# Optimization experiments

Measured on AMD Instinct MI355X. Metric: run time of the kernel, lower is better.

Reference implementation:

```python
import jax, jax.numpy as jnp
import numpy as np

B = 32      # batch
N = 1024    # input_size (= maxval)
EPS = 1.0   # regularization_strength


def _isotonic_l2(y):
    """Non-increasing isotonic regression (L2) of each row of y: [B, n].

    Uses the minimax characterization  sol_i = min_{j<=i} max_{k>=i} mean(y[j..k]),
    which equals the PAV solution and yields the correct block-averaging Jacobian
    under autodiff. O(n^2) memory per row, fully vectorized.
    """
    b, n = y.shape
    cs = jnp.concatenate([jnp.zeros((b, 1), y.dtype), jnp.cumsum(y, axis=-1)], axis=-1)  # [B, n+1]
    j = jnp.arange(n)[:, None]   # start index
    k = jnp.arange(n)[None, :]   # end index
    length = (k - j + 1).astype(y.dtype)
    # M[b, j, k] = mean(y[b, j..k]) for k >= j
    M = (cs[:, None, 1:] - cs[:, :-1, None]) / jnp.where(k >= j, length, jnp.ones_like(length))
    M = jnp.where(k >= j, M, -jnp.inf)
    # Amax[b, j, i] = max_{k >= i} M[b, j, k]  (suffix max along k)
    Amax = jax.lax.cummax(M, axis=2, reverse=True)
    # restrict to j <= i, then minimize over j
    Amax = jnp.where(j <= k, Amax, jnp.inf)  # here the k-axis plays the role of i
    return jnp.min(Amax, axis=1)  # [B, n]


def _soft_rank(x, eps):
    """fast-soft-sort soft_rank, direction=ASCENDING, regularization='l2'."""
    b, n = x.shape
    theta = x / eps
    perm = jnp.argsort(-theta, axis=-1)                 # descending sort permutation
    s = jnp.take_along_axis(theta, perm, axis=-1)       # sorted (descending)
    w = jnp.arange(n, 0, -1, dtype=x.dtype)             # [n, n-1, ..., 1]
    sol = _isotonic_l2(s - w)                           # dual solution
    primal = s - sol                                    # projection, sorted order
    inv = jnp.argsort(perm, axis=-1)
    return jnp.take_along_axis(primal, inv, axis=-1)    # unpermute -> ranks in [1, n]


def setup_inputs() -> dict:
    key = jax.random.key(0)
    x = jax.random.normal(key, (B, N), dtype=jnp.float32)
    return {"x": x}


def reference(x) -> jnp.ndarray:
    ranks = _soft_rank(x, EPS)                          # [B, n]
    n = x.shape[1]
    t = jnp.arange(1, n + 1, dtype=x.dtype)             # rank targets 1..n
    # out[b, j, i] = relu(1 - |ranks[b, j] - (i + 1)|)  (== torch .permute(0, 2, 1) result)
    return jax.nn.relu(1.0 - jnp.abs(ranks[:, :, None] - t[None, None, :]))
```

## Files before the change

### kernel.cpp

```cpp
#include <hip/hip_runtime.h>
#include <stdint.h>

#define N 1024
#define BATCH 32
#define NFILL 2048

__global__ __launch_bounds__(256) void fused_kernel(const float* __restrict__ x,
                                                    float* __restrict__ out,
                                                    float* __restrict__ ranks) {
    if (blockIdx.x >= BATCH) {
        const int fid = blockIdx.x - BATCH;
        float4* o = reinterpret_cast<float4*>(out) + (size_t)fid * 4096 + threadIdx.x;
        const float4 z = make_float4(0.0f, 0.0f, 0.0f, 0.0f);
        #pragma unroll
        for (int i = 0; i < 16; ++i)
            o[i * 256] = z;
        return;
    }

    __shared__ double   regA[N];
    __shared__ float    regB[N];
    __shared__ uint16_t segid[N];
    __shared__ uint16_t run_start[N+1];
    __shared__ double   stk_sum[N];
    __shared__ uint32_t stk_cr[N];
    __shared__ double   wsumD[4];
    __shared__ int      wsumI[4];

    uint64_t* keys     = reinterpret_cast<uint64_t*>(regA);
    double*   csum     = regA;
    float*    ss       = regB;
    float*    yv       = regB;
    float*    run_mean = regB;

    const int b = blockIdx.x;
    const int t = threadIdx.x;
    const int j0 = t << 2;
    const int lane = t & 63;
    const int wid = t >> 6;

    const float4 xq = reinterpret_cast<const float4*>(x + b * N)[t];
    const float vv[4] = {xq.x, xq.y, xq.z, xq.w};
    uint64_t kk[4];
    {
        #pragma unroll
        for (int e = 0; e < 4; ++e) {
            uint32_t u = __float_as_uint(vv[e]);
            u ^= (u & 0x80000000u) ? 0xFFFFFFFFu : 0x80000000u;
            kk[e] = (((uint64_t)u) << 10) | (uint64_t)(1023 - (j0 + e));
            keys[j0 + e] = kk[e];
        }
    }
    __syncthreads();

    int c[4] = {0, 0, 0, 0};
    for (int k = 0; k < N; k += 4) {
        const uint64_t k0 = keys[k];
        const uint64_t k1 = keys[k + 1];
        const uint64_t k2 = keys[k + 2];
        const uint64_t k3 = keys[k + 3];
        #pragma unroll
        for (int e = 0; e < 4; ++e) {
            c[e] += (int)(k0 > kk[e]);
            c[e] += (int)(k1 > kk[e]);
            c[e] += (int)(k2 > kk[e]);
            c[e] += (int)(k3 > kk[e]);
        }
    }
    __syncthreads();
    ss[c[0]] = xq.x; ss[c[1]] = xq.y; ss[c[2]] = xq.z; ss[c[3]] = xq.w;
    __syncthreads();

    float4 yq;
    {
        const float4 sq = reinterpret_cast<const float4*>(ss)[t];
        yq.x = sq.x + (float)(j0 - 512);
        yq.y = sq.y + (float)(j0 - 511);
        yq.z = sq.z + (float)(j0 - 510);
        yq.w = sq.w + (float)(j0 - 509);
        reinterpret_cast<float4*>(yv)[t] = yq;
    }
    __syncthreads();

    const float ye[4] = {yq.x, yq.y, yq.z, yq.w};
    int    fl[4];
    int    lf[4];
    double lys[4];
    {
        float prev = (j0 == 0) ? -1.0e30f : yv[j0 - 1];
        double accy = 0.0; int accf = 0;
        #pragma unroll
        for (int e = 0; e < 4; ++e) {
            const int f = (prev > ye[e]) ? 1 : 0;
            prev = ye[e];
            fl[e] = f;
            accf += f;             lf[e]  = accf;
            accy += (double)ye[e]; lys[e] = accy;
        }
    }
    double vy = lys[3]; int vf = lf[3];
    #pragma unroll
    for (int off = 1; off < 64; off <<= 1) {
        const double oy = __shfl_up(vy, off);
        const int    of = __shfl_up(vf, off);
        if (lane >= off) { vy += oy; vf += of; }
    }
    if (lane == 63) { wsumD[wid] = vy; wsumI[wid] = vf; }
    __syncthreads();
    {
        double basey = vy - lys[3]; int basef = vf - lf[3];
        for (int w = 0; w < wid; ++w) { basey += wsumD[w]; basef += wsumI[w]; }
        #pragma unroll
        for (int e = 0; e < 4; ++e) {
            const int p   = j0 + e;
            const int seg = basef + lf[e];
            segid[p] = (uint16_t)seg;
            csum[p]  = basey + lys[e];
            if (fl[e]) run_start[seg] = (uint16_t)p;
        }
        if (t == 0) run_start[0] = 0;
    }
    __syncthreads();

    if (t == 0) {
        const int R = (int)segid[N - 1] + 1;
        run_start[R] = (uint16_t)N;
        int sp = 0;
        for (int r = 0; r < R; ++r) {
            const int a   = (int)run_start[r];
            const int bnd = (int)run_start[r + 1];
            double s = csum[bnd - 1] - ((a > 0) ? csum[a - 1] : 0.0);
            int    cc = bnd - a;
            int    nr = 1;
            while (sp > 0) {
                const uint32_t cr  = stk_cr[sp - 1];
                const int      tc  = (int)(cr & 0xFFFFu);
                if (!(s * (double)tc > stk_sum[sp - 1] * (double)cc)) break;
                s  += stk_sum[sp - 1];
                cc += tc;
                nr += (int)(cr >> 16);
                --sp;
            }
            stk_sum[sp] = s;
            stk_cr[sp]  = (uint32_t)cc | ((uint32_t)nr << 16);
            ++sp;
        }
        int rc = 0;
        for (int e2 = 0; e2 < sp; ++e2) {
            const uint32_t cr = stk_cr[e2];
            const float m = (float)(stk_sum[e2] / (double)(cr & 0xFFFFu));
            const int   nr = (int)(cr >> 16);
            for (int q2 = 0; q2 < nr; ++q2) run_mean[rc++] = m;
        }
    }
    __syncthreads();

    float4 r4;
    r4.x = vv[0] - run_mean[segid[c[0]]] + 512.0f;
    r4.y = vv[1] - run_mean[segid[c[1]]] + 512.0f;
    r4.z = vv[2] - run_mean[segid[c[2]]] + 512.0f;
    r4.w = vv[3] - run_mean[segid[c[3]]] + 512.0f;
    reinterpret_cast<float4*>(ranks + b * N)[t] = r4;
}

__global__ __launch_bounds__(256) void scatter_kernel(const float* __restrict__ ranks,
                                                      float* __restrict__ out) {
    const int row = blockIdx.x * 256 + threadIdx.x;
    const float r = ranks[row];
    const float f = floorf(r);
    const int   i1 = (int)f;
    const float frac = r - f;
    float* o = out + (size_t)row * N;
    if (i1 >= 1 && i1 <= N) o[i1 - 1] = 1.0f - frac;
    if (i1 >= 0 && i1 <  N) o[i1]     = frac;
}

extern "C" void kernel_launch(void* const* d_in, const int* in_sizes, int n_in,
                              void* d_out, int out_size, void* d_ws, size_t ws_size,
                              hipStream_t stream) {
    const float* x = (const float*)d_in[0];
    float* out = (float*)d_out;
    float* ranks = (float*)d_ws;

    fused_kernel<<<BATCH + NFILL, 256, 0, stream>>>(x, out, ranks);
    scatter_kernel<<<(BATCH * N) / 256, 256, 0, stream>>>(ranks, out);
}
```

Measured before the change: 141.0 us.

## Fuse scatter into fill blocks via global atomic counter spin-wait

Removes the separate scatter kernel launch. Fill blocks now zero a contiguous range of 27 rows each, then spin on a global counter until all 32 rank-computing blocks have signalled, then scatter their own rows' two nonzero values. A tiny init kernel resets the counter. This trades a kernel boundary for an in-kernel spin barrier. That barrier relies on all rank blocks being co-resident, and the fill-block spin could delay them.

```diff
diff --git a/kernel.cpp b/kernel.cpp
--- a/kernel.cpp
+++ b/kernel.cpp
@@ -3,18 +3,51 @@
 
 #define N 1024
 #define BATCH 32
-#define NFILL 2048
+#define NFILL 1216
+#define ROWS_PER_FILL 27
+#define TOTROWS (BATCH * N)
+
+__global__ __launch_bounds__(64) void init_kernel(int* __restrict__ counter) {
+    if (threadIdx.x == 0) *counter = 0;
+}
 
 __global__ __launch_bounds__(256) void fused_kernel(const float* __restrict__ x,
                                                     float* __restrict__ out,
-                                                    float* __restrict__ ranks) {
+                                                    float* __restrict__ ranks,
+                                                    int* __restrict__ counter) {
+    const int t = threadIdx.x;
+
     if (blockIdx.x >= BATCH) {
-        const int fid = blockIdx.x - BATCH;
-        float4* o = reinterpret_cast<float4*>(out) + (size_t)fid * 4096 + threadIdx.x;
+        const int fid   = blockIdx.x - BATCH;
+        const int rb    = fid * ROWS_PER_FILL;
+        const int nrows = min(ROWS_PER_FILL, TOTROWS - rb);
+        if (nrows <= 0) return;
+
+        float4* o = reinterpret_cast<float4*>(out) + (size_t)rb * 256 + t;
         const float4 z = make_float4(0.0f, 0.0f, 0.0f, 0.0f);
-        #pragma unroll
-        for (int i = 0; i < 16; ++i)
-            o[i * 256] = z;
+        #pragma unroll 4
+        for (int k = 0; k < nrows; ++k)
+            o[k * 256] = z;
+
+        __syncthreads();
+
+        if (t == 0) {
+            while (__hip_atomic_load(counter, __ATOMIC_ACQUIRE,
+                                     __HIP_MEMORY_SCOPE_AGENT) < BATCH)
+                __builtin_amdgcn_s_sleep(32);
+        }
+        __syncthreads();
+
+        if (t < nrows) {
+            const int   row  = rb + t;
+            const float r    = ranks[row];
+            const float f    = floorf(r);
+            const int   i1   = (int)f;
+            const float frac = r - f;
+            float* orow = out + (size_t)row * N;
+            if (i1 >= 1 && i1 <= N) orow[i1 - 1] = 1.0f - frac;
+            if (i1 >= 0 && i1 <  N) orow[i1]     = frac;
+        }
         return;
     }
 
@@ -34,7 +67,6 @@
     float*    run_mean = regB;
 
     const int b = blockIdx.x;
-    const int t = threadIdx.x;
     const int j0 = t << 2;
     const int lane = t & 63;
     const int wid = t >> 6;
@@ -161,18 +193,11 @@
     r4.z = vv[2] - run_mean[segid[c[2]]] + 512.0f;
     r4.w = vv[3] - run_mean[segid[c[3]]] + 512.0f;
     reinterpret_cast<float4*>(ranks + b * N)[t] = r4;
-}
-
-__global__ __launch_bounds__(256) void scatter_kernel(const float* __restrict__ ranks,
-                                                      float* __restrict__ out) {
-    const int row = blockIdx.x * 256 + threadIdx.x;
-    const float r = ranks[row];
-    const float f = floorf(r);
-    const int   i1 = (int)f;
-    const float frac = r - f;
-    float* o = out + (size_t)row * N;
-    if (i1 >= 1 && i1 <= N) o[i1 - 1] = 1.0f - frac;
-    if (i1 >= 0 && i1 <  N) o[i1]     = frac;
+
+    __syncthreads();
+    if (t == 0)
+        __hip_atomic_fetch_add(counter, 1, __ATOMIC_RELEASE,
+                               __HIP_MEMORY_SCOPE_AGENT);
 }
 
 extern "C" void kernel_launch(void* const* d_in, const int* in_sizes, int n_in,
@@ -181,7 +206,8 @@
     const float* x = (const float*)d_in[0];
     float* out = (float*)d_out;
     float* ranks = (float*)d_ws;
-
-    fused_kernel<<<BATCH + NFILL, 256, 0, stream>>>(x, out, ranks);
-    scatter_kernel<<<(BATCH * N) / 256, 256, 0, stream>>>(ranks, out);
+    int* counter = (int*)((float*)d_ws + TOTROWS + 16);
+
+    init_kernel<<<1, 64, 0, stream>>>(counter);
+    fused_kernel<<<BATCH + NFILL, 256, 0, stream>>>(x, out, ranks, counter);
 }
```

New measurement: 169.8 us. 20.4% more time.
